# Performance work log

Hardware: AMD Instinct MI355X
Metric: run time of the kernel (lower is better)

The kernel has to match this reference:

```python
import math
import jax, jax.numpy as jnp
import numpy as np

N = 2048          # batch size
D = 256           # embedding_dim
MEM = 16384       # memory_size
ANOMALY_WEIGHT = 1.0
TEMP = 0.1
MOMENTUM = 0.01
NCLS = 2          # binary phishing labels -> max(labels.max()+1, 2) == 2


def setup_inputs() -> dict:
    key = jax.random.key(0)
    ks = jax.random.split(key, 10)
    s = 1.0 / math.sqrt(D)  # nn.Linear default init range
    return {
        'z': jax.random.normal(ks[0], (N, D), jnp.float32),
        'labels': jax.random.randint(ks[1], (N,), 0, NCLS),
        'memory': jax.random.normal(ks[2], (MEM, D), jnp.float32),
        'memory_weights': jax.random.uniform(ks[3], (MEM,), jnp.float32),
        'running_mean': jnp.zeros((D,), jnp.float32),
        'running_cov': jnp.eye(D, dtype=jnp.float32),
        'Wq': jax.random.uniform(ks[4], (D, D), jnp.float32, -s, s),
        'bq': jax.random.uniform(ks[5], (D,), jnp.float32, -s, s),
        'Wk': jax.random.uniform(ks[6], (D, D), jnp.float32, -s, s),
        'bk': jax.random.uniform(ks[7], (D,), jnp.float32, -s, s),
        'Wv': jax.random.uniform(ks[8], (D, D), jnp.float32, -s, s),
        'bv': jax.random.uniform(ks[9], (D,), jnp.float32, -s, s),
    }


def reference(z, labels, memory, memory_weights, running_mean, running_cov,
              Wq, bq, Wk, bk, Wv, bv):
    # ---- update(z.detach(), labels): entire update path is detached in torch ----
    z_sg = jax.lax.stop_gradient(z)

    # _update_stats: EMA of batch mean / covariance (done before importance)
    mu = z_sg.mean(axis=0)                                  # [D]
    zc = z_sg - mu
    cov = zc.T @ zc / max(N - 1, 1)                         # [D, D]
    rm = (1.0 - MOMENTUM) * running_mean + MOMENTUM * mu
    rc = (1.0 - MOMENTUM) * running_cov + MOMENTUM * cov

    # _mahalanobis with updated running stats
    c = z_sg - rm
    cov_inv = jnp.linalg.inv(rc + 1e-6 * jnp.eye(D, dtype=rc.dtype))
    dist = jnp.sqrt(jnp.clip(jnp.einsum('nd,de,ne->n', c, cov_inv, c), 1e-8))
    a_norm = (dist - dist.min()) / (dist.max() - dist.min() + 1e-8)

    # _mi_proxy: KL(batch label dist || uniform), broadcast to all items
    counts = jnp.zeros((NCLS,), z.dtype).at[labels].add(1.0)
    p = counts / jnp.clip(counts.sum(), 1.0)
    # p / uniform == p * NCLS; clip inside log for safety (both classes present)
    kl = jnp.clip((p * jnp.log(jnp.clip(p * NCLS, 1e-8))).sum(), 0.0)
    importance = (1.0 + ANOMALY_WEIGHT * a_norm) * kl       # [N]

    # serial top-1 priority-queue eviction, in descending-importance order
    order = jnp.argsort(-importance)
    z_ord = z_sg[order]
    imp_ord = importance[order]

    def evict_step(state, inp):
        mem, w = state
        zi, imp = inp
        j = jnp.argmin(w)                   # weakest memory slot
        rep = imp > w[j]
        mem = mem.at[j].set(jnp.where(rep, zi, mem[j]))
        w = w.at[j].set(jnp.where(rep, imp, w[j]))
        return (mem, w), None

    (mem, _), _ = jax.lax.scan(evict_step, (memory, memory_weights), (z_ord, imp_ord))

    # ---- query(z): cross-attention over the (full) updated memory ----
    Q = z @ Wq.T + bq                       # [N, D]
    K = mem @ Wk.T + bk                     # [MEM, D]
    V = mem @ Wv.T + bv                     # [MEM, D]
    sc = (Q @ K.T) / math.sqrt(D)           # [N, MEM]
    attn = jax.nn.softmax(sc / TEMP, axis=-1)
    return z + 0.5 * (attn @ V)
```

## Files before the change

kernel.cpp:

```cpp
#include <hip/hip_runtime.h>
#include <math.h>

#define NB   2048
#define DE   256
#define MEMN 16384
#define CAND_CAP 256
#define FSPL 32
#define FKPS 512
#define FIT  16

typedef __attribute__((ext_vector_type(8)))  short  short8;
typedef __attribute__((ext_vector_type(16))) float  float16;
typedef __attribute__((ext_vector_type(4)))  unsigned uint4v;
typedef __attribute__((ext_vector_type(2)))  unsigned uint2v;

static const size_t OFF_QB   = 0;
static const size_t OFF_KB   = 262144;
static const size_t OFF_VTB  = 2359296;
static const size_t OFF_LP   = 4456448;
static const size_t OFF_OPB  = 4521984;
static const size_t SO_A    = 0;
static const size_t SO_MUP  = 131072;
static const size_t SO_DIST = 147456;

__device__ inline unsigned short f2bf(float f) {
  unsigned u = __float_as_uint(f);
  unsigned r = (u + 0x7fffu + ((u >> 16) & 1u)) >> 16;
  return (unsigned short)r;
}
__device__ inline float bf2f(unsigned short s) {
  return __uint_as_float((unsigned)s << 16);
}

__device__ inline unsigned cvtpk_bf16(float lo, float hi) {
  unsigned r;
  asm("v_cvt_pk_bf16_f32 %0, %1, %2" : "=v"(r) : "v"(lo), "v"(hi));
  return r;
}
__device__ inline short8 pack8_bf16(float4 f0, float4 f1) {
  uint4v u = {cvtpk_bf16(f0.x, f0.y), cvtpk_bf16(f0.z, f0.w),
              cvtpk_bf16(f1.x, f1.y), cvtpk_bf16(f1.z, f1.w)};
  return __builtin_bit_cast(short8, u);
}

__device__ inline void halfswap(unsigned& lo, unsigned& hi, int h) {
#if __has_builtin(__builtin_amdgcn_permlane32_swap)
  (void)h;
  uint2v r = __builtin_amdgcn_permlane32_swap(lo, hi, false, false);
  lo = r.x; hi = r.y;
#else
  unsigned a = (unsigned)__shfl_xor((int)lo, 32, 64);
  unsigned b = (unsigned)__shfl_xor((int)hi, 32, 64);
  unsigned nlo = (h == 0) ? lo : b;
  unsigned nhi = (h == 0) ? a  : hi;
  lo = nlo; hi = nhi;
#endif
}

__device__ inline void bitonic_sort_u64(unsigned long long* key, int n, int tid, int nth) {
  for (int k = 2; k <= n; k <<= 1) {
    for (int j = k >> 1; j > 0; j >>= 1) {
      __syncthreads();
      for (int i = tid; i < n; i += nth) {
        int ixj = i ^ j;
        if (ixj > i) {
          unsigned long long a = key[i], b = key[ixj];
          bool up = ((i & k) == 0);
          if ((a > b) == up) { key[i] = b; key[ixj] = a; }
        }
      }
    }
  }
  __syncthreads();
}

__global__ __launch_bounds__(256) void covmu_kernel(const float* __restrict__ z,
                                                    float* __restrict__ A,
                                                    float* __restrict__ mup) {
  int f = blockIdx.x;
  int tid = threadIdx.x;
  if (f >= 256) {
    int b = f - 256;
    int r0 = b * 32;
    float s = 0.f;
    for (int r = 0; r < 32; ++r) s += z[(size_t)(r0 + r) * DE + tid];
    mup[b * DE + tid] = s;
    return;
  }
  __shared__ float As[16][68];
  __shared__ float Bs[16][68];
  int tx = tid & 15, ty = tid >> 4;
  int i0 = (f & 3) * 64, j0 = ((f >> 2) & 3) * 64;
  int nbase = (f >> 4) * 128;
  float acc[4][4] = {};
  for (int nt = 0; nt < 8; ++nt) {
    int n0 = nbase + nt * 16;
    for (int e = tid; e < 1024; e += 256) {
      int c = e & 63, nn = e >> 6;
      As[nn][c] = z[(size_t)(n0 + nn) * DE + i0 + c];
      Bs[nn][c] = z[(size_t)(n0 + nn) * DE + j0 + c];
    }
    __syncthreads();
#pragma unroll
    for (int nn = 0; nn < 16; ++nn) {
      float4 a4 = *(const float4*)&As[nn][ty * 4];
      float4 b4 = *(const float4*)&Bs[nn][tx * 4];
      acc[0][0] += a4.x*b4.x; acc[0][1] += a4.x*b4.y; acc[0][2] += a4.x*b4.z; acc[0][3] += a4.x*b4.w;
      acc[1][0] += a4.y*b4.x; acc[1][1] += a4.y*b4.y; acc[1][2] += a4.y*b4.z; acc[1][3] += a4.y*b4.w;
      acc[2][0] += a4.z*b4.x; acc[2][1] += a4.z*b4.y; acc[2][2] += a4.z*b4.z; acc[2][3] += a4.z*b4.w;
      acc[3][0] += a4.w*b4.x; acc[3][1] += a4.w*b4.y; acc[3][2] += a4.w*b4.z; acc[3][3] += a4.w*b4.w;
    }
    __syncthreads();
  }
  for (int r = 0; r < 4; ++r) {
    int i = i0 + ty * 4 + r;
    for (int c = 0; c < 4; ++c) {
      int j = j0 + tx * 4 + c;
      atomicAdd(&A[(size_t)i * DE + j], acc[r][c]);
    }
  }
}

__global__ __launch_bounds__(256) void dist_kernel(const float* __restrict__ z,
                                                   const float* __restrict__ rmean,
                                                   const float* __restrict__ mup,
                                                   const float* __restrict__ ZtZ,
                                                   const float* __restrict__ rcov,
                                                   float* __restrict__ dist) {
  __shared__ float cc[8][256];
  __shared__ float mus[256];
  __shared__ float4 red[256];
  int n0 = blockIdx.x * 8, i = threadIdx.x;
  float s = 0.f;
  for (int b = 0; b < 64; ++b) s += mup[b * DE + i];
  mus[i] = s;
  float rmi = 0.99f * rmean[i] + 0.01f * s * (1.0f / (float)NB);
#pragma unroll
  for (int r = 0; r < 8; ++r) cc[r][i] = z[(size_t)(n0 + r) * DE + i] - rmi;
  __syncthreads();
  const float c1 = 0.01f / (float)(NB - 1);
  const float invN = 1.0f / (float)NB;
  float musi = mus[i];
  float u[8] = {};
#pragma unroll 4
  for (int j = 0; j < DE; ++j) {
    float base = 0.99f * rcov[(size_t)j * DE + i] +
                 c1 * (ZtZ[(size_t)j * DE + i] - mus[j] * musi * invN);
    float e = -base;
    if (j == i) e += 1.0f - 1e-6f;
#pragma unroll
    for (int r = 0; r < 8; ++r) u[r] += e * cc[r][j];
  }
  {
    float4 v;
    v.x = cc[0][i] * (cc[0][i] + u[0]) + u[0] * u[0];
    v.y = cc[1][i] * (cc[1][i] + u[1]) + u[1] * u[1];
    v.z = cc[2][i] * (cc[2][i] + u[2]) + u[2] * u[2];
    v.w = cc[3][i] * (cc[3][i] + u[3]) + u[3] * u[3];
    red[i] = v;
    __syncthreads();
    for (int sH = 128; sH > 0; sH >>= 1) {
      if (i < sH) {
        float4 a = red[i], b = red[i + sH];
        a.x += b.x; a.y += b.y; a.z += b.z; a.w += b.w;
        red[i] = a;
      }
      __syncthreads();
    }
    if (i < 4) {
      float4 tt = red[0];
      float d = (i == 0) ? tt.x : (i == 1) ? tt.y : (i == 2) ? tt.z : tt.w;
      dist[n0 + i] = sqrtf(fmaxf(d, 1e-8f));
    }
    __syncthreads();
  }
  {
    float4 v;
    v.x = cc[4][i] * (cc[4][i] + u[4]) + u[4] * u[4];
    v.y = cc[5][i] * (cc[5][i] + u[5]) + u[5] * u[5];
    v.z = cc[6][i] * (cc[6][i] + u[6]) + u[6] * u[6];
    v.w = cc[7][i] * (cc[7][i] + u[7]) + u[7] * u[7];
    red[i] = v;
    __syncthreads();
    for (int sH = 128; sH > 0; sH >>= 1) {
      if (i < sH) {
        float4 a = red[i], b = red[i + sH];
        a.x += b.x; a.y += b.y; a.z += b.z; a.w += b.w;
        red[i] = a;
      }
      __syncthreads();
    }
    if (i < 4) {
      float4 tt = red[0];
      float d = (i == 0) ? tt.x : (i == 1) ? tt.y : (i == 2) ? tt.z : tt.w;
      dist[n0 + 4 + i] = sqrtf(fmaxf(d, 1e-8f));
    }
  }
}

__global__ __launch_bounds__(1024) void update_kernel(const float* __restrict__ dist,
                                                      const int* __restrict__ labels,
                                                      const float* __restrict__ weights,
                                                      const float* __restrict__ z,
                                                      float* __restrict__ memory) {
  __shared__ unsigned long long ikeys[NB];
  __shared__ unsigned long long ck[CAND_CAP];
  __shared__ unsigned long long gmin[16];
  __shared__ int slots[CAND_CAP], srcs[CAND_CAP];
  __shared__ float smin[16], smax[16];
  __shared__ int scnt[16];
  __shared__ float s_kl, s_dmin, s_inv;
  __shared__ int s_ccnt, s_m, s_stop, s_bg;
  int t = threadIdx.x;
  int wid = t >> 6, lane = t & 63;

  float mn = 1e30f, mx = -1e30f; int c1 = 0;
  for (int n = t; n < NB; n += 1024) {
    float d = dist[n];
    mn = fminf(mn, d); mx = fmaxf(mx, d);
    c1 += labels[n];
  }
#pragma unroll
  for (int o = 32; o > 0; o >>= 1) {
    mn = fminf(mn, __shfl_xor(mn, o, 64));
    mx = fmaxf(mx, __shfl_xor(mx, o, 64));
    c1 += __shfl_xor(c1, o, 64);
  }
  if (lane == 0) { smin[wid] = mn; smax[wid] = mx; scnt[wid] = c1; }
  if (t == 0) { s_ccnt = 0; s_m = 0; s_stop = 0; }
  __syncthreads();
  if (t == 0) {
    float a = 1e30f, b = -1e30f; int cc = 0;
    for (int i = 0; i < 16; ++i) { a = fminf(a, smin[i]); b = fmaxf(b, smax[i]); cc += scnt[i]; }
    float p1 = (float)cc / (float)NB;
    float p0 = (float)(NB - cc) / (float)NB;
    float kl = p0 * logf(fmaxf(2.f * p0, 1e-8f)) + p1 * logf(fmaxf(2.f * p1, 1e-8f));
    s_kl = fmaxf(kl, 0.f);
    s_dmin = a;
    s_inv = 1.0f / (b - a + 1e-8f);
  }
  __syncthreads();
  float kl = s_kl;

  for (int n = t; n < NB; n += 1024) {
    float imp = (1.0f + (dist[n] - s_dmin) * s_inv) * kl;
    ikeys[n] = ((unsigned long long)(unsigned)(~__float_as_uint(imp)) << 32) | (unsigned)n;
  }
  float thresh = 2.f * kl;
  for (int j = t; j < MEMN; j += 1024) {
    float wv = weights[j];
    if (wv < thresh) {
      int p = atomicAdd(&s_ccnt, 1);
      if (p < CAND_CAP) ck[p] = ((unsigned long long)__float_as_uint(wv) << 32) | (unsigned)j;
    }
  }
  __syncthreads();
  int C = s_ccnt; if (C > CAND_CAP) C = CAND_CAP;
  for (int i = t; i < CAND_CAP; i += 1024)
    if (i >= C) ck[i] = 0xFFFFFFFFFFFFFFFFULL;
  __syncthreads();
  if (C <= 64) {
    if (wid == 0) {
      unsigned long long key = (lane < C) ? ck[lane] : 0xFFFFFFFFFFFFFFFFULL;
      int rank = 0;
      for (int j = 0; j < 64; ++j) {
        unsigned long long o = (unsigned long long)__shfl((long long)key, j, 64);
        rank += (o < key) || (o == key && j < lane);
      }
      if (lane < C) ck[rank] = key;
    }
    __syncthreads();
  } else {
    bitonic_sort_u64(ck, CAND_CAP, t, 1024);
  }

  {
    unsigned long long a = ikeys[wid * 128 + lane];
    unsigned long long b = ikeys[wid * 128 + 64 + lane];
    unsigned long long mm = a < b ? a : b;
#pragma unroll
    for (int o = 32; o > 0; o >>= 1) {
      unsigned long long ot = (unsigned long long)__shfl_xor((long long)mm, o, 64);
      if (ot < mm) mm = ot;
    }
    if (lane == 0) gmin[wid] = mm;
  }
  __syncthreads();

  float prevv = 0.f;
  for (int i = 0; i < C; ++i) {
    if (t == 0) {
      unsigned long long best = 0xFFFFFFFFFFFFFFFFULL;
      for (int g = 0; g < 16; ++g) if (gmin[g] < best) best = gmin[g];
      float im = __uint_as_float(~(unsigned)(best >> 32));
      float wv = __uint_as_float((unsigned)(ck[i] >> 32));
      bool ok = (im > wv) && (i == 0 || prevv >= wv);
      if (ok) {
        int idx = (int)(best & 0xffffffffULL);
        slots[s_m] = (int)(ck[i] & 0xffffffffULL);
        srcs[s_m]  = idx;
        s_m++;
        prevv = im;
        ikeys[idx] = 0xFFFFFFFFFFFFFFFFULL;
        s_bg = idx >> 7;
      } else {
        s_stop = 1; s_bg = -1;
      }
    }
    __syncthreads();
    if (s_stop) break;
    if (wid == s_bg) {
      unsigned long long a = ikeys[wid * 128 + lane];
      unsigned long long b = ikeys[wid * 128 + 64 + lane];
      unsigned long long mm = a < b ? a : b;
#pragma unroll
      for (int o = 32; o > 0; o >>= 1) {
        unsigned long long ot = (unsigned long long)__shfl_xor((long long)mm, o, 64);
        if (ot < mm) mm = ot;
      }
      if (lane == 0) gmin[wid] = mm;
    }
    __syncthreads();
  }
  int m = s_m;
  for (int e = t; e < m * DE; e += 1024) {
    int i = e >> 8, d = e & 255;
    memory[(size_t)slots[i] * DE + d] = z[(size_t)srcs[i] * DE + d];
  }
}

__global__ __launch_bounds__(256, 1) void qkv_kernel(
    const float* __restrict__ z, const float* __restrict__ memory,
    const float* __restrict__ Wq, const float* __restrict__ bq,
    const float* __restrict__ Wk, const float* __restrict__ bk,
    const float* __restrict__ Wv, const float* __restrict__ bv,
    unsigned short* __restrict__ Qbf, unsigned short* __restrict__ Kbf,
    unsigned short* __restrict__ Vtb) {
  __shared__ unsigned short Bsh[64 * 264];
  int flat = blockIdx.x;
  int tid = threadIdx.x;
  int w = tid >> 6, lane = tid & 63;
  int m = lane & 31, h = lane >> 5;

  if (flat < 64) {
    int gx = flat & 15, gy = flat >> 4;
    int arow = gx * 128 + w * 32 + m;
    int n0 = gy * 64;
    short8 af[16];
#pragma unroll
    for (int kc = 0; kc < 16; ++kc) {
      const float* src = &z[(size_t)arow * DE + kc * 16 + h * 8];
      af[kc] = pack8_bf16(*(const float4*)&src[0], *(const float4*)&src[4]);
    }
    {
      int r = tid >> 2, q = tid & 3;
      const float* src = &Wq[(size_t)(n0 + r) * DE + q * 64];
      unsigned short* dst = &Bsh[r * 264 + q * 64];
#pragma unroll
      for (int j = 0; j < 8; ++j)
        *(short8*)&dst[j * 8] = pack8_bf16(*(const float4*)&src[j * 8],
                                           *(const float4*)&src[j * 8 + 4]);
    }
    __syncthreads();
    float16 a0 = {}, a1 = {};
#pragma unroll
    for (int kc = 0; kc < 16; ++kc) {
      short8 b0 = *(const short8*)&Bsh[(0 * 32 + m) * 264 + kc * 16 + h * 8];
      short8 b1 = *(const short8*)&Bsh[(1 * 32 + m) * 264 + kc * 16 + h * 8];
      a0 = __builtin_amdgcn_mfma_f32_32x32x16_bf16(af[kc], b0, a0, 0, 0, 0);
      a1 = __builtin_amdgcn_mfma_f32_32x32x16_bf16(af[kc], b1, a1, 0, 0, 0);
    }
#pragma unroll
    for (int r = 0; r < 16; ++r) {
      int rr = (r & 3) + 8 * (r >> 2) + 4 * h;
      int orow = gx * 128 + w * 32 + rr;
      int oc0 = n0 + m, oc1 = n0 + 32 + m;
      Qbf[(size_t)orow * DE + oc0] = f2bf(a0[r] + bq[oc0]);
      Qbf[(size_t)orow * DE + oc1] = f2bf(a1[r] + bq[oc1]);
    }
  } else if (flat < 192) {
    int gx = flat - 64;
    int arow = gx * 128 + w * 32 + m;
    short8 af[16];
#pragma unroll
    for (int kc = 0; kc < 16; ++kc) {
      const float* src = &memory[(size_t)arow * DE + kc * 16 + h * 8];
      af[kc] = pack8_bf16(*(const float4*)&src[0], *(const float4*)&src[4]);
    }
    for (int g4 = 0; g4 < 4; ++g4) {
      int n0 = g4 * 64;
      __syncthreads();
      {
        int r = tid >> 2, q = tid & 3;
        const float* src = &Wk[(size_t)(n0 + r) * DE + q * 64];
        unsigned short* dst = &Bsh[r * 264 + q * 64];
#pragma unroll
        for (int j = 0; j < 8; ++j)
          *(short8*)&dst[j * 8] = pack8_bf16(*(const float4*)&src[j * 8],
                                             *(const float4*)&src[j * 8 + 4]);
      }
      __syncthreads();
      float16 a0 = {}, a1 = {};
#pragma unroll
      for (int kc = 0; kc < 16; ++kc) {
        short8 b0 = *(const short8*)&Bsh[(0 * 32 + m) * 264 + kc * 16 + h * 8];
        short8 b1 = *(const short8*)&Bsh[(1 * 32 + m) * 264 + kc * 16 + h * 8];
        a0 = __builtin_amdgcn_mfma_f32_32x32x16_bf16(af[kc], b0, a0, 0, 0, 0);
        a1 = __builtin_amdgcn_mfma_f32_32x32x16_bf16(af[kc], b1, a1, 0, 0, 0);
      }
#pragma unroll
      for (int r = 0; r < 16; ++r) {
        int rr = (r & 3) + 8 * (r >> 2) + 4 * h;
        int orow = gx * 128 + w * 32 + rr;
        int oc0 = n0 + m, oc1 = n0 + 32 + m;
        Kbf[(size_t)orow * DE + oc0] = f2bf(a0[r] + bk[oc0]);
        Kbf[(size_t)orow * DE + oc1] = f2bf(a1[r] + bk[oc1]);
      }
    }
  } else {
    int gy = flat - 192;
    int n0 = gy * 64;
    {
      int r = tid >> 2, q = tid & 3;
      const float* src = &memory[(size_t)(n0 + r) * DE + q * 64];
      unsigned short* dst = &Bsh[r * 264 + q * 64];
#pragma unroll
      for (int j = 0; j < 8; ++j)
        *(short8*)&dst[j * 8] = pack8_bf16(*(const float4*)&src[j * 8],
                                           *(const float4*)&src[j * 8 + 4]);
    }
    __syncthreads();
    for (int gxv = 0; gxv < 2; ++gxv) {
      short8 af[16];
#pragma unroll
      for (int kc = 0; kc < 16; ++kc) {
        const float* src = &Wv[(size_t)(gxv * 128 + w * 32 + m) * DE + kc * 16 + h * 8];
        af[kc] = pack8_bf16(*(const float4*)&src[0], *(const float4*)&src[4]);
      }
      float16 a0 = {}, a1 = {};
#pragma unroll
      for (int kc = 0; kc < 16; ++kc) {
        short8 b0 = *(const short8*)&Bsh[(0 * 32 + m) * 264 + kc * 16 + h * 8];
        short8 b1 = *(const short8*)&Bsh[(1 * 32 + m) * 264 + kc * 16 + h * 8];
        a0 = __builtin_amdgcn_mfma_f32_32x32x16_bf16(af[kc], b0, a0, 0, 0, 0);
        a1 = __builtin_amdgcn_mfma_f32_32x32x16_bf16(af[kc], b1, a1, 0, 0, 0);
      }
#pragma unroll
      for (int r = 0; r < 16; ++r) {
        int rr = (r & 3) + 8 * (r >> 2) + 4 * h;
        int orow = gxv * 128 + w * 32 + rr;
        int oc0 = n0 + m, oc1 = n0 + 32 + m;
        Vtb[(size_t)(oc0 >> 5) * 8192 + (size_t)orow * 32 + (oc0 & 31)] = f2bf(a0[r] + bv[orow]);
        Vtb[(size_t)(oc1 >> 5) * 8192 + (size_t)orow * 32 + (oc1 & 31)] = f2bf(a1[r] + bv[orow]);
      }
    }
  }
}

__global__ __launch_bounds__(512, 2) void flash_kernel(
    const unsigned short* __restrict__ Qb, const unsigned short* __restrict__ Kb,
    const unsigned short* __restrict__ Vtb, unsigned short* __restrict__ Opb,
    float* __restrict__ Lp) {
  __shared__ unsigned short Ks[32 * 264];
  __shared__ unsigned short Vs[256 * 40];

  int tid = threadIdx.x;
  int w = tid >> 6, lane = tid & 63;
  int m = lane & 31, h = lane >> 5;
  int sp = blockIdx.x, qg = blockIdx.y;
  int myrow = qg * 256 + w * 32 + m;

  short8 qf[16];
#pragma unroll
  for (int kc = 0; kc < 16; ++kc)
    qf[kc] = *(const short8*)&Qb[(size_t)myrow * DE + kc * 16 + h * 8];

  float16 O[8] = {};
  float lacc = 0.f;

  short8 kreg[2], vreg[2];
#define LOAD_TILES(kb_)                                                              \
  {                                                                                  \
    int kb = (kb_);                                                                  \
    _Pragma("unroll")                                                                \
    for (int i = 0; i < 2; ++i) {                                                    \
      int c = i * 512 + tid, kr = c >> 5, kcol = c & 31;                             \
      kreg[i] = *(const short8*)&Kb[(size_t)(kb + kr) * DE + kcol * 8];              \
    }                                                                                \
    const unsigned short* vg = &Vtb[(size_t)((kb) >> 5) * 8192];                     \
    _Pragma("unroll")                                                                \
    for (int i = 0; i < 2; ++i) {                                                    \
      int c = i * 512 + tid;                                                         \
      vreg[i] = *(const short8*)&vg[c * 8];                                          \
    }                                                                                \
  }
#define STORE_TILES()                                                                \
  {                                                                                  \
    _Pragma("unroll")                                                                \
    for (int i = 0; i < 2; ++i) {                                                    \
      int c = i * 512 + tid, kr = c >> 5, kcol = c & 31;                             \
      *(short8*)&Ks[kr * 264 + kcol * 8] = kreg[i];                                  \
    }                                                                                \
    _Pragma("unroll")                                                                \
    for (int i = 0; i < 2; ++i) {                                                    \
      int c = i * 512 + tid, dr = c >> 2, dc = c & 3;                                \
      *(short8*)&Vs[dr * 40 + dc * 8] = vreg[i];                                     \
    }                                                                                \
  }

  LOAD_TILES(sp * FKPS);

  for (int it = 0; it < FIT; ++it) {
    __syncthreads();
    STORE_TILES();
    if (it + 1 < FIT) LOAD_TILES(sp * FKPS + (it + 1) * 32);
    __syncthreads();

    float16 s = {};
    __builtin_amdgcn_s_setprio(1);
#pragma unroll
    for (int kc = 0; kc < 16; ++kc) {
      short8 b0 = *(const short8*)&Ks[m * 264 + kc * 16 + h * 8];
      s = __builtin_amdgcn_mfma_f32_32x32x16_bf16(b0, qf[kc], s, 0, 0, 0);
    }
    __builtin_amdgcn_s_setprio(0);

    float p[16];
#pragma unroll
    for (int r = 0; r < 16; ++r)
      p[r] = exp2f(fmaf(s[r], 0.90168440f, -16.0f));

    lacc += ((p[0] + p[1]) + (p[2] + p[3])) + ((p[4] + p[5]) + (p[6] + p[7])) +
            ((p[8] + p[9]) + (p[10] + p[11])) + ((p[12] + p[13]) + (p[14] + p[15]));

    unsigned c0 = cvtpk_bf16(p[0],  p[1]);
    unsigned c1 = cvtpk_bf16(p[2],  p[3]);
    unsigned c2 = cvtpk_bf16(p[4],  p[5]);
    unsigned c3 = cvtpk_bf16(p[6],  p[7]);
    unsigned c4 = cvtpk_bf16(p[8],  p[9]);
    unsigned c5 = cvtpk_bf16(p[10], p[11]);
    unsigned c6 = cvtpk_bf16(p[12], p[13]);
    unsigned c7 = cvtpk_bf16(p[14], p[15]);
    halfswap(c0, c2, h);
    halfswap(c1, c3, h);
    halfswap(c4, c6, h);
    halfswap(c5, c7, h);
    uint4v w0v = {c0, c1, c2, c3};
    uint4v w1v = {c4, c5, c6, c7};
    short8 pa0 = __builtin_bit_cast(short8, w0v);
    short8 pa1 = __builtin_bit_cast(short8, w1v);

    __builtin_amdgcn_s_setprio(1);
#pragma unroll
    for (int ct = 0; ct < 8; ++ct) {
      short8 vb0 = *(const short8*)&Vs[(ct * 32 + m) * 40 + h * 8];
      short8 vb1 = *(const short8*)&Vs[(ct * 32 + m) * 40 + 16 + h * 8];
      O[ct] = __builtin_amdgcn_mfma_f32_32x32x16_bf16(pa0, vb0, O[ct], 0, 0, 0);
      O[ct] = __builtin_amdgcn_mfma_f32_32x32x16_bf16(pa1, vb1, O[ct], 0, 0, 0);
    }
    __builtin_amdgcn_s_setprio(0);
  }
#undef LOAD_TILES
#undef STORE_TILES

  size_t ob = ((size_t)sp * NB + qg * 256 + w * 32) * DE;
#pragma unroll
  for (int ct = 0; ct < 8; ++ct)
#pragma unroll
    for (int r = 0; r < 16; ++r) {
      int rr = (r & 3) + 8 * (r >> 2) + 4 * h;
      Opb[ob + (size_t)rr * DE + ct * 32 + m] = f2bf(O[ct][r]);
    }
  float ltot = lacc + __shfl_xor(lacc, 32, 64);
  if (h == 0)
    Lp[sp * NB + qg * 256 + w * 32 + m] = ltot;
}

__global__ __launch_bounds__(256) void combine_kernel(const float* __restrict__ z,
                                                      const unsigned short* __restrict__ Opb,
                                                      const float* __restrict__ Lp,
                                                      float* __restrict__ out) {
  int t = threadIdx.x;
  int n = blockIdx.x * 8 + (t >> 5);
  int c0 = (t & 31) * 8;
  float num[8] = {};
  float den = 0.f;
#pragma unroll
  for (int s = 0; s < FSPL; ++s) {
    den += Lp[s * NB + n];
    short8 v = *(const short8*)&Opb[((size_t)s * NB + n) * DE + c0];
#pragma unroll
    for (int j = 0; j < 8; ++j) num[j] += bf2f((unsigned short)v[j]);
  }
  size_t base = (size_t)n * DE + c0;
  float4 o0, o1;
  o0.x = z[base + 0] + 0.5f * num[0] / den;
  o0.y = z[base + 1] + 0.5f * num[1] / den;
  o0.z = z[base + 2] + 0.5f * num[2] / den;
  o0.w = z[base + 3] + 0.5f * num[3] / den;
  o1.x = z[base + 4] + 0.5f * num[4] / den;
  o1.y = z[base + 5] + 0.5f * num[5] / den;
  o1.z = z[base + 6] + 0.5f * num[6] / den;
  o1.w = z[base + 7] + 0.5f * num[7] / den;
  *(float4*)&out[base] = o0;
  *(float4*)&out[base + 4] = o1;
}

extern "C" void kernel_launch(void* const* d_in, const int* in_sizes, int n_in,
                              void* d_out, int out_size, void* d_ws, size_t ws_size,
                              hipStream_t stream) {
  (void)in_sizes; (void)n_in; (void)out_size; (void)ws_size;
  const float* z       = (const float*)d_in[0];
  const int*   labels  = (const int*)d_in[1];
  float*       memory  = (float*)d_in[2];
  const float* weights = (const float*)d_in[3];
  const float* rmean   = (const float*)d_in[4];
  const float* rcov    = (const float*)d_in[5];
  const float* Wq      = (const float*)d_in[6];
  const float* bq      = (const float*)d_in[7];
  const float* Wk      = (const float*)d_in[8];
  const float* bk      = (const float*)d_in[9];
  const float* Wv      = (const float*)d_in[10];
  const float* bv      = (const float*)d_in[11];
  float* out = (float*)d_out;
  float* ws  = (float*)d_ws;

  unsigned short* Qbf = (unsigned short*)(ws + OFF_QB);
  unsigned short* Kbf = (unsigned short*)(ws + OFF_KB);
  unsigned short* Vtb = (unsigned short*)(ws + OFF_VTB);
  float* Lp           = ws + OFF_LP;
  unsigned short* Opb = (unsigned short*)(ws + OFF_OPB);
  float* SB    = ws + OFF_OPB;
  float* A     = SB + SO_A;
  float* mup   = SB + SO_MUP;
  float* dist  = SB + SO_DIST;

  hipMemsetAsync(A, 0, (size_t)DE * DE * sizeof(float), stream);
  covmu_kernel<<<320, 256, 0, stream>>>(z, A, mup);
  dist_kernel<<<NB / 8, 256, 0, stream>>>(z, rmean, mup, A, rcov, dist);
  update_kernel<<<1, 1024, 0, stream>>>(dist, labels, weights, z, memory);
  qkv_kernel<<<448, 256, 0, stream>>>(z, memory, Wq, bq, Wk, bk, Wv, bv, Qbf, Kbf, Vtb);
  flash_kernel<<<dim3(FSPL, NB / 256), 512, 0, stream>>>(Qbf, Kbf, Vtb, Opb, Lp);
  combine_kernel<<<NB / 8, 256, 0, stream>>>(z, Opb, Lp, out);
}
```

Before: 226.9 us.

## Replace covariance atomics with partial buffers and move Q projection earlier

Each covariance tile block now writes its partial sum to its own slice buffer instead of using atomicAdd into a zeroed matrix, and a new small reduction kernel sums the 16 slices. This removes the memset and the atomic contention. The Q projection, which depends only on z, moves from the post-update qkv kernel into the first covmu launch, so it overlaps with the covariance blocks and shortens the qkv launch. In exchange it adds a kernel launch and about 4MB of extra partial-buffer traffic.

```diff
diff --git a/kernel.cpp b/kernel.cpp
--- a/kernel.cpp
+++ b/kernel.cpp
@@ -19,9 +19,10 @@
 static const size_t OFF_VTB  = 2359296;
 static const size_t OFF_LP   = 4456448;
 static const size_t OFF_OPB  = 4521984;
-static const size_t SO_A    = 0;
-static const size_t SO_MUP  = 131072;
-static const size_t SO_DIST = 147456;
+static const size_t SO_APART = 0;
+static const size_t SO_A     = 1048576;
+static const size_t SO_MUP   = 1114112;
+static const size_t SO_DIST  = 1130496;
 
 __device__ inline unsigned short f2bf(float f) {
   unsigned u = __float_as_uint(f);
@@ -75,10 +76,55 @@
 }
 
 __global__ __launch_bounds__(256) void covmu_kernel(const float* __restrict__ z,
-                                                    float* __restrict__ A,
-                                                    float* __restrict__ mup) {
+                                                    float* __restrict__ Apart,
+                                                    float* __restrict__ mup,
+                                                    const float* __restrict__ Wq,
+                                                    const float* __restrict__ bq,
+                                                    unsigned short* __restrict__ Qbf) {
   int f = blockIdx.x;
   int tid = threadIdx.x;
+  if (f >= 320) {
+    __shared__ unsigned short Bsh[64 * 264];
+    int g = f - 320;
+    int gx = g & 15, gy = g >> 4;
+    int w = tid >> 6, lane = tid & 63;
+    int m = lane & 31, h = lane >> 5;
+    int arow = gx * 128 + w * 32 + m;
+    int n0 = gy * 64;
+    short8 af[16];
+#pragma unroll
+    for (int kc = 0; kc < 16; ++kc) {
+      const float* src = &z[(size_t)arow * DE + kc * 16 + h * 8];
+      af[kc] = pack8_bf16(*(const float4*)&src[0], *(const float4*)&src[4]);
+    }
+    {
+      int r = tid >> 2, q = tid & 3;
+      const float* src = &Wq[(size_t)(n0 + r) * DE + q * 64];
+      unsigned short* dst = &Bsh[r * 264 + q * 64];
+#pragma unroll
+      for (int j = 0; j < 8; ++j)
+        *(short8*)&dst[j * 8] = pack8_bf16(*(const float4*)&src[j * 8],
+                                           *(const float4*)&src[j * 8 + 4]);
+    }
+    __syncthreads();
+    float16 a0 = {}, a1 = {};
+#pragma unroll
+    for (int kc = 0; kc < 16; ++kc) {
+      short8 b0 = *(const short8*)&Bsh[(0 * 32 + m) * 264 + kc * 16 + h * 8];
+      short8 b1 = *(const short8*)&Bsh[(1 * 32 + m) * 264 + kc * 16 + h * 8];
+      a0 = __builtin_amdgcn_mfma_f32_32x32x16_bf16(af[kc], b0, a0, 0, 0, 0);
+      a1 = __builtin_amdgcn_mfma_f32_32x32x16_bf16(af[kc], b1, a1, 0, 0, 0);
+    }
+#pragma unroll
+    for (int r = 0; r < 16; ++r) {
+      int rr = (r & 3) + 8 * (r >> 2) + 4 * h;
+      int orow = gx * 128 + w * 32 + rr;
+      int oc0 = n0 + m, oc1 = n0 + 32 + m;
+      Qbf[(size_t)orow * DE + oc0] = f2bf(a0[r] + bq[oc0]);
+      Qbf[(size_t)orow * DE + oc1] = f2bf(a1[r] + bq[oc1]);
+    }
+    return;
+  }
   if (f >= 256) {
     int b = f - 256;
     int r0 = b * 32;
@@ -91,7 +137,8 @@
   __shared__ float Bs[16][68];
   int tx = tid & 15, ty = tid >> 4;
   int i0 = (f & 3) * 64, j0 = ((f >> 2) & 3) * 64;
-  int nbase = (f >> 4) * 128;
+  int slice = f >> 4;
+  int nbase = slice * 128;
   float acc[4][4] = {};
   for (int nt = 0; nt < 8; ++nt) {
     int n0 = nbase + nt * 16;
@@ -112,13 +159,26 @@
     }
     __syncthreads();
   }
+  float* dstA = &Apart[(size_t)slice * 65536];
   for (int r = 0; r < 4; ++r) {
     int i = i0 + ty * 4 + r;
     for (int c = 0; c < 4; ++c) {
       int j = j0 + tx * 4 + c;
-      atomicAdd(&A[(size_t)i * DE + j], acc[r][c]);
-    }
-  }
+      dstA[(size_t)i * DE + j] = acc[r][c];
+    }
+  }
+}
+
+__global__ __launch_bounds__(256) void covred_kernel(const float* __restrict__ Apart,
+                                                     float* __restrict__ A) {
+  int e0 = (blockIdx.x * 256 + threadIdx.x) * 4;
+  float4 s = {0.f, 0.f, 0.f, 0.f};
+#pragma unroll
+  for (int sl = 0; sl < 16; ++sl) {
+    float4 v = *(const float4*)&Apart[(size_t)sl * 65536 + e0];
+    s.x += v.x; s.y += v.y; s.z += v.z; s.w += v.w;
+  }
+  *(float4*)&A[e0] = s;
 }
 
 __global__ __launch_bounds__(256) void dist_kernel(const float* __restrict__ z,
@@ -330,56 +390,18 @@
 }
 
 __global__ __launch_bounds__(256, 1) void qkv_kernel(
-    const float* __restrict__ z, const float* __restrict__ memory,
-    const float* __restrict__ Wq, const float* __restrict__ bq,
+    const float* __restrict__ memory,
     const float* __restrict__ Wk, const float* __restrict__ bk,
     const float* __restrict__ Wv, const float* __restrict__ bv,
-    unsigned short* __restrict__ Qbf, unsigned short* __restrict__ Kbf,
-    unsigned short* __restrict__ Vtb) {
+    unsigned short* __restrict__ Kbf, unsigned short* __restrict__ Vtb) {
   __shared__ unsigned short Bsh[64 * 264];
   int flat = blockIdx.x;
   int tid = threadIdx.x;
   int w = tid >> 6, lane = tid & 63;
   int m = lane & 31, h = lane >> 5;
 
-  if (flat < 64) {
-    int gx = flat & 15, gy = flat >> 4;
-    int arow = gx * 128 + w * 32 + m;
-    int n0 = gy * 64;
-    short8 af[16];
-#pragma unroll
-    for (int kc = 0; kc < 16; ++kc) {
-      const float* src = &z[(size_t)arow * DE + kc * 16 + h * 8];
-      af[kc] = pack8_bf16(*(const float4*)&src[0], *(const float4*)&src[4]);
-    }
-    {
-      int r = tid >> 2, q = tid & 3;
-      const float* src = &Wq[(size_t)(n0 + r) * DE + q * 64];
-      unsigned short* dst = &Bsh[r * 264 + q * 64];
-#pragma unroll
-      for (int j = 0; j < 8; ++j)
-        *(short8*)&dst[j * 8] = pack8_bf16(*(const float4*)&src[j * 8],
-                                           *(const float4*)&src[j * 8 + 4]);
-    }
-    __syncthreads();
-    float16 a0 = {}, a1 = {};
-#pragma unroll
-    for (int kc = 0; kc < 16; ++kc) {
-      short8 b0 = *(const short8*)&Bsh[(0 * 32 + m) * 264 + kc * 16 + h * 8];
-      short8 b1 = *(const short8*)&Bsh[(1 * 32 + m) * 264 + kc * 16 + h * 8];
-      a0 = __builtin_amdgcn_mfma_f32_32x32x16_bf16(af[kc], b0, a0, 0, 0, 0);
-      a1 = __builtin_amdgcn_mfma_f32_32x32x16_bf16(af[kc], b1, a1, 0, 0, 0);
-    }
-#pragma unroll
-    for (int r = 0; r < 16; ++r) {
-      int rr = (r & 3) + 8 * (r >> 2) + 4 * h;
-      int orow = gx * 128 + w * 32 + rr;
-      int oc0 = n0 + m, oc1 = n0 + 32 + m;
-      Qbf[(size_t)orow * DE + oc0] = f2bf(a0[r] + bq[oc0]);
-      Qbf[(size_t)orow * DE + oc1] = f2bf(a1[r] + bq[oc1]);
-    }
-  } else if (flat < 192) {
-    int gx = flat - 64;
+  if (flat < 128) {
+    int gx = flat;
     int arow = gx * 128 + w * 32 + m;
     short8 af[16];
 #pragma unroll
@@ -418,7 +440,7 @@
       }
     }
   } else {
-    int gy = flat - 192;
+    int gy = flat - 128;
     int n0 = gy * 64;
     {
       int r = tid >> 2, q = tid & 3;
@@ -631,15 +653,16 @@
   float* Lp           = ws + OFF_LP;
   unsigned short* Opb = (unsigned short*)(ws + OFF_OPB);
   float* SB    = ws + OFF_OPB;
+  float* Apart = SB + SO_APART;
   float* A     = SB + SO_A;
   float* mup   = SB + SO_MUP;
   float* dist  = SB + SO_DIST;
 
-  hipMemsetAsync(A, 0, (size_t)DE * DE * sizeof(float), stream);
-  covmu_kernel<<<320, 256, 0, stream>>>(z, A, mup);
+  covmu_kernel<<<384, 256, 0, stream>>>(z, Apart, mup, Wq, bq, Qbf);
+  covred_kernel<<<64, 256, 0, stream>>>(Apart, A);
   dist_kernel<<<NB / 8, 256, 0, stream>>>(z, rmean, mup, A, rcov, dist);
   update_kernel<<<1, 1024, 0, stream>>>(dist, labels, weights, z, memory);
-  qkv_kernel<<<448, 256, 0, stream>>>(z, memory, Wq, bq, Wk, bk, Wv, bv, Qbf, Kbf, Vtb);
+  qkv_kernel<<<384, 256, 0, stream>>>(memory, Wk, bk, Wv, bv, Kbf, Vtb);
   flash_kernel<<<dim3(FSPL, NB / 256), 512, 0, stream>>>(Qbf, Kbf, Vtb, Opb, Lp);
   combine_kernel<<<NB / 8, 256, 0, stream>>>(z, Opb, Lp, out);
 }
```

Result: faster. 215.5 us, median of 2 (-5.0%).
